# Kernel tuning notes

Measured on AMD Instinct MI355X. Metric: run time of the kernel, lower is better.

The kernel has to match this reference:

```python
import jax, jax.numpy as jnp
import numpy as np

LN_EPS = 1e-5


def _layernorm_2d(x, w, b):
    # LayerNorm over the last two dims (d, d) with elementwise affine.
    mu = jnp.mean(x, axis=(-2, -1), keepdims=True)
    var = jnp.var(x, axis=(-2, -1), keepdims=True)
    return (x - mu) * jax.lax.rsqrt(var + LN_EPS) * w + b


def setup_inputs() -> dict:
    key = jax.random.key(0)
    k_x, k_a, k_w, k_b = jax.random.split(key, 4)
    B, T, D = 2, 512, 64
    x = jax.random.normal(k_x, (B, T, D, D), dtype=jnp.float32)
    log_A = jax.random.normal(k_a, (D,), dtype=jnp.float32) * 0.02
    # dt_proj: nn.Linear(dim, 1) -> weight (1, dim) stored here as (dim,), bias (1,)
    bound = 1.0 / np.sqrt(D)
    dt_w = jax.random.uniform(k_w, (D,), dtype=jnp.float32, minval=-bound, maxval=bound)
    dt_b = jax.random.uniform(k_b, (1,), dtype=jnp.float32, minval=-bound, maxval=bound)
    ln_w = jnp.ones((D, D), dtype=jnp.float32)
    ln_b = jnp.zeros((D, D), dtype=jnp.float32)
    return {"x": x, "log_A": log_A, "dt_w": dt_w, "dt_b": dt_b, "ln_w": ln_w, "ln_b": ln_b}


def reference(x, log_A, dt_w, dt_b, ln_w, ln_b):
    B, T, D, _ = x.shape
    xn = _layernorm_2d(x, ln_w, ln_b)                          # [B,T,D,D]
    A_cont = -jnp.exp(log_A)                                   # [D]
    dt = jax.nn.softplus(jnp.einsum('btrc,c->btr', xn, dt_w) + dt_b)  # [B,T,D]
    log_decay = dt * A_cont                                    # [B,T,D]
    cs = jnp.cumsum(log_decay, axis=1)                         # [B,T,D]
    log_M = cs[:, :, None, :] - cs[:, None, :, :]              # [B,T,T,D]
    idx = jnp.arange(T)
    causal = (idx[:, None] >= idx[None, :])[None, :, :, None]  # [1,T,T,1]
    M = jnp.exp(jnp.where(causal, log_M, -jnp.inf))            # [B,T,T,D]
    out = jnp.einsum('btjr,bjrc->btrc', M, xn)                 # [B,T,D,D]
    return out
```

## Files before the change

kernel.cpp:

```cpp
#include <hip/hip_runtime.h>
#include <math.h>

#define B_SZ 2
#define T_SZ 512
#define D_SZ 64
#define ELEMS 4096

#define NCH2 64
#define CLEN2 8
#define NCG  16

#define DECAY_BYTES ((size_t)B_SZ * D_SZ * T_SZ * 4)
#define M_OFF   DECAY_BYTES
#define R_OFF   (DECAY_BYTES + (size_t)B_SZ * T_SZ * 4)

__global__ __launch_bounds__(256) void ln_dt_kernel(
    const float* __restrict__ x, const float* __restrict__ log_A,
    const float* __restrict__ dt_w, const float* __restrict__ dt_b,
    const float* __restrict__ ln_w, const float* __restrict__ ln_b,
    float* __restrict__ decay_t, float* __restrict__ Mst, float* __restrict__ Rst)
{
    const int bt  = blockIdx.x;
    const int tid = threadIdx.x;
    const size_t base = (size_t)bt * ELEMS;

    float4 v[4];
    float sum = 0.f, sumsq = 0.f;
    const float4* xv4 = reinterpret_cast<const float4*>(x + base);
#pragma unroll
    for (int k = 0; k < 4; ++k) {
        v[k] = xv4[tid + 256 * k];
        sum   += v[k].x + v[k].y + v[k].z + v[k].w;
        sumsq += v[k].x * v[k].x + v[k].y * v[k].y + v[k].z * v[k].z + v[k].w * v[k].w;
    }

    __shared__ float red0[4], red1[4];
#pragma unroll
    for (int off = 32; off; off >>= 1) {
        sum   += __shfl_down(sum, off);
        sumsq += __shfl_down(sumsq, off);
    }
    const int wave = tid >> 6;
    if ((tid & 63) == 0) { red0[wave] = sum; red1[wave] = sumsq; }
    __syncthreads();
    sum   = red0[0] + red0[1] + red0[2] + red0[3];
    sumsq = red1[0] + red1[1] + red1[2] + red1[3];

    const float mu = sum * (1.f / ELEMS);
    const float var = sumsq * (1.f / ELEMS) - mu * mu;
    const float rs = rsqrtf(var + 1e-5f);

    const float4* w4p = reinterpret_cast<const float4*>(ln_w);
    const float4* b4p = reinterpret_cast<const float4*>(ln_b);
    const float4* dw4 = reinterpret_cast<const float4*>(dt_w);
    float dot[4] = {0.f, 0.f, 0.f, 0.f};
#pragma unroll
    for (int k = 0; k < 4; ++k) {
        const int f = tid + 256 * k;
        float4 w4 = w4p[f];
        float4 b4 = b4p[f];
        float4 xn;
        xn.x = (v[k].x - mu) * rs * w4.x + b4.x;
        xn.y = (v[k].y - mu) * rs * w4.y + b4.y;
        xn.z = (v[k].z - mu) * rs * w4.z + b4.z;
        xn.w = (v[k].w - mu) * rs * w4.w + b4.w;
        float4 wv = dw4[f & 15];
        dot[k] += xn.x * wv.x + xn.y * wv.y + xn.z * wv.z + xn.w * wv.w;
    }

#pragma unroll
    for (int m = 1; m <= 8; m <<= 1) {
#pragma unroll
        for (int k = 0; k < 4; ++k) dot[k] += __shfl_xor(dot[k], m);
    }

    if (tid == 0) { Mst[bt] = mu * rs; Rst[bt] = rs; }

    if ((tid & 15) == 0) {
        const int m = tid >> 4;
        const float db = dt_b[0];
        const int b = bt >> 9;
        const int t = bt & (T_SZ - 1);
#pragma unroll
        for (int k = 0; k < 4; ++k) {
            const int r = m + 16 * k;
            const float z = dot[k] + db;
            const float dt = (z > 20.f) ? z : log1pf(expf(z));
            const float A = -expf(log_A[r]);
            decay_t[((size_t)(b * D_SZ + r)) * T_SZ + t] = expf(dt * A);
        }
    }
}

__global__ __launch_bounds__(1024, 1) void scan_row4_kernel(
    const float* __restrict__ x,
    const float* __restrict__ Mst, const float* __restrict__ Rst,
    const float* __restrict__ decay_t,
    const float* __restrict__ ln_w, const float* __restrict__ ln_b,
    float* __restrict__ out)
{
    const int tid = threadIdx.x;
    const int cg  = tid & (NCG - 1);
    const int k   = tid >> 4;
    const int b   = blockIdx.x >> 6;
    const int r   = blockIdx.x & 63;
    const int t0  = k * CLEN2;
    const int c0  = cg * 4;

    __shared__ float  sd[T_SZ];
    __shared__ float  sM[T_SZ];
    __shared__ float  sR[T_SZ];
    __shared__ float4 sS[NCH2][NCG];
    __shared__ float  sP[NCH2];

    if (tid < 128) {
        reinterpret_cast<float4*>(sd)[tid] =
            reinterpret_cast<const float4*>(decay_t + (size_t)blockIdx.x * T_SZ)[tid];
    } else if (tid < 256) {
        const int i = tid - 128;
        reinterpret_cast<float4*>(sM)[i] =
            reinterpret_cast<const float4*>(Mst + b * T_SZ)[i];
    } else if (tid < 384) {
        const int i = tid - 256;
        reinterpret_cast<float4*>(sR)[i] =
            reinterpret_cast<const float4*>(Rst + b * T_SZ)[i];
    }
    const float4 lw = *reinterpret_cast<const float4*>(ln_w + r * D_SZ + c0);
    const float4 lb = *reinterpret_cast<const float4*>(ln_b + r * D_SZ + c0);
    __syncthreads();

    const float* xp = x + ((size_t)(b * T_SZ + t0) * D_SZ + r) * D_SZ + c0;

    float4 v[CLEN2];
    float4 S = make_float4(0.f, 0.f, 0.f, 0.f);
    float  P = 1.f;
#pragma unroll
    for (int i = 0; i < CLEN2; ++i) {
        const float4 xv = *reinterpret_cast<const float4*>(xp + (size_t)i * ELEMS);
        const int   t = t0 + i;
        const float M = sM[t], R = sR[t], d = sd[t];
        const float xn0 = fmaf(fmaf(xv.x, R, -M), lw.x, lb.x);
        const float xn1 = fmaf(fmaf(xv.y, R, -M), lw.y, lb.y);
        const float xn2 = fmaf(fmaf(xv.z, R, -M), lw.z, lb.z);
        const float xn3 = fmaf(fmaf(xv.w, R, -M), lw.w, lb.w);
        S.x = fmaf(S.x, d, xn0);
        S.y = fmaf(S.y, d, xn1);
        S.z = fmaf(S.z, d, xn2);
        S.w = fmaf(S.w, d, xn3);
        P *= d;
        v[i] = S;
    }

    sS[k][cg] = S;
    if (cg == 0) sP[k] = P;
    __syncthreads();

    float4 C = make_float4(0.f, 0.f, 0.f, 0.f);
    for (int j = 0; j < k; ++j) {
        const float  Pj = sP[j];
        const float4 Sj = sS[j][cg];
        C.x = fmaf(Pj, C.x, Sj.x);
        C.y = fmaf(Pj, C.y, Sj.y);
        C.z = fmaf(Pj, C.z, Sj.z);
        C.w = fmaf(Pj, C.w, Sj.w);
    }

    float* op = out + ((size_t)(b * T_SZ + t0) * D_SZ + r) * D_SZ + c0;
    float rp = 1.f;
#pragma unroll
    for (int i = 0; i < CLEN2; ++i) {
        rp *= sd[t0 + i];
        float4 o;
        o.x = fmaf(rp, C.x, v[i].x);
        o.y = fmaf(rp, C.y, v[i].y);
        o.z = fmaf(rp, C.z, v[i].z);
        o.w = fmaf(rp, C.w, v[i].w);
        *reinterpret_cast<float4*>(op + (size_t)i * ELEMS) = o;
    }
}

extern "C" void kernel_launch(void* const* d_in, const int* in_sizes, int n_in,
                              void* d_out, int out_size, void* d_ws, size_t ws_size,
                              hipStream_t stream) {
    const float* x     = (const float*)d_in[0];
    const float* log_A = (const float*)d_in[1];
    const float* dt_w  = (const float*)d_in[2];
    const float* dt_b  = (const float*)d_in[3];
    const float* ln_w  = (const float*)d_in[4];
    const float* ln_b  = (const float*)d_in[5];
    float* out     = (float*)d_out;
    float* decay_t = (float*)d_ws;
    float* Mst     = (float*)((char*)d_ws + M_OFF);
    float* Rst     = (float*)((char*)d_ws + R_OFF);

    ln_dt_kernel<<<B_SZ * T_SZ, 256, 0, stream>>>(
        x, log_A, dt_w, dt_b, ln_w, ln_b, decay_t, Mst, Rst);

    scan_row4_kernel<<<B_SZ * D_SZ, 1024, 0, stream>>>(
        x, Mst, Rst, decay_t, ln_w, ln_b, out);
}
```

Measured before the change: 23.41 us.

## Move dt/decay computation into scan kernel; reduce first kernel to stats only

The first kernel now only computes per-(b,t) LayerNorm mean and rstd, with no ln_w/ln_b/dt_w loads and no decay writes. The scan kernel normalizes x itself, computes the dt dot product with a 16-lane shuffle reduction, applies softplus and exp to get the decay per row, and keeps decays in registers. The x loads are also hoisted ahead of the shared-memory staging so they overlap. This removes the decay workspace round trip and shrinks the first pass, at the cost of extra transcendental and shuffle work inside the latency-bound scan kernel.

```diff
diff --git a/kernel.cpp b/kernel.cpp
--- a/kernel.cpp
+++ b/kernel.cpp
@@ -10,92 +10,51 @@
 #define CLEN2 8
 #define NCG  16
 
-#define DECAY_BYTES ((size_t)B_SZ * D_SZ * T_SZ * 4)
-#define M_OFF   DECAY_BYTES
-#define R_OFF   (DECAY_BYTES + (size_t)B_SZ * T_SZ * 4)
+#define M_OFF 0
+#define R_OFF ((size_t)B_SZ * T_SZ * 4)
 
-__global__ __launch_bounds__(256) void ln_dt_kernel(
-    const float* __restrict__ x, const float* __restrict__ log_A,
-    const float* __restrict__ dt_w, const float* __restrict__ dt_b,
-    const float* __restrict__ ln_w, const float* __restrict__ ln_b,
-    float* __restrict__ decay_t, float* __restrict__ Mst, float* __restrict__ Rst)
+__global__ __launch_bounds__(256) void stats_kernel(
+    const float* __restrict__ x,
+    float* __restrict__ Mst, float* __restrict__ Rst)
 {
     const int bt  = blockIdx.x;
     const int tid = threadIdx.x;
     const size_t base = (size_t)bt * ELEMS;
 
-    float4 v[4];
-    float sum = 0.f, sumsq = 0.f;
+    float sum = 0.f, ssq = 0.f;
     const float4* xv4 = reinterpret_cast<const float4*>(x + base);
 #pragma unroll
     for (int k = 0; k < 4; ++k) {
-        v[k] = xv4[tid + 256 * k];
-        sum   += v[k].x + v[k].y + v[k].z + v[k].w;
-        sumsq += v[k].x * v[k].x + v[k].y * v[k].y + v[k].z * v[k].z + v[k].w * v[k].w;
+        const float4 v = xv4[tid + 256 * k];
+        sum += v.x + v.y + v.z + v.w;
+        ssq += v.x * v.x + v.y * v.y + v.z * v.z + v.w * v.w;
     }
 
     __shared__ float red0[4], red1[4];
 #pragma unroll
     for (int off = 32; off; off >>= 1) {
-        sum   += __shfl_down(sum, off);
-        sumsq += __shfl_down(sumsq, off);
+        sum += __shfl_down(sum, off);
+        ssq += __shfl_down(ssq, off);
     }
     const int wave = tid >> 6;
-    if ((tid & 63) == 0) { red0[wave] = sum; red1[wave] = sumsq; }
+    if ((tid & 63) == 0) { red0[wave] = sum; red1[wave] = ssq; }
     __syncthreads();
-    sum   = red0[0] + red0[1] + red0[2] + red0[3];
-    sumsq = red1[0] + red1[1] + red1[2] + red1[3];
-
-    const float mu = sum * (1.f / ELEMS);
-    const float var = sumsq * (1.f / ELEMS) - mu * mu;
-    const float rs = rsqrtf(var + 1e-5f);
-
-    const float4* w4p = reinterpret_cast<const float4*>(ln_w);
-    const float4* b4p = reinterpret_cast<const float4*>(ln_b);
-    const float4* dw4 = reinterpret_cast<const float4*>(dt_w);
-    float dot[4] = {0.f, 0.f, 0.f, 0.f};
-#pragma unroll
-    for (int k = 0; k < 4; ++k) {
-        const int f = tid + 256 * k;
-        float4 w4 = w4p[f];
-        float4 b4 = b4p[f];
-        float4 xn;
-        xn.x = (v[k].x - mu) * rs * w4.x + b4.x;
-        xn.y = (v[k].y - mu) * rs * w4.y + b4.y;
-        xn.z = (v[k].z - mu) * rs * w4.z + b4.z;
-        xn.w = (v[k].w - mu) * rs * w4.w + b4.w;
-        float4 wv = dw4[f & 15];
-        dot[k] += xn.x * wv.x + xn.y * wv.y + xn.z * wv.z + xn.w * wv.w;
-    }
-
-#pragma unroll
-    for (int m = 1; m <= 8; m <<= 1) {
-#pragma unroll
-        for (int k = 0; k < 4; ++k) dot[k] += __shfl_xor(dot[k], m);
-    }
-
-    if (tid == 0) { Mst[bt] = mu * rs; Rst[bt] = rs; }
-
-    if ((tid & 15) == 0) {
-        const int m = tid >> 4;
-        const float db = dt_b[0];
-        const int b = bt >> 9;
-        const int t = bt & (T_SZ - 1);
-#pragma unroll
-        for (int k = 0; k < 4; ++k) {
-            const int r = m + 16 * k;
-            const float z = dot[k] + db;
-            const float dt = (z > 20.f) ? z : log1pf(expf(z));
-            const float A = -expf(log_A[r]);
-            decay_t[((size_t)(b * D_SZ + r)) * T_SZ + t] = expf(dt * A);
-        }
+    if (tid == 0) {
+        sum = red0[0] + red0[1] + red0[2] + red0[3];
+        ssq = red1[0] + red1[1] + red1[2] + red1[3];
+        const float mu = sum * (1.f / ELEMS);
+        const float var = ssq * (1.f / ELEMS) - mu * mu;
+        const float rs = rsqrtf(var + 1e-5f);
+        Mst[bt] = mu * rs;
+        Rst[bt] = rs;
     }
 }
 
-__global__ __launch_bounds__(1024, 1) void scan_row4_kernel(
+__global__ __launch_bounds__(1024, 1) void scan_full_kernel(
     const float* __restrict__ x,
     const float* __restrict__ Mst, const float* __restrict__ Rst,
-    const float* __restrict__ decay_t,
+    const float* __restrict__ log_A,
+    const float* __restrict__ dt_w, const float* __restrict__ dt_b,
     const float* __restrict__ ln_w, const float* __restrict__ ln_b,
     float* __restrict__ out)
 {
@@ -107,47 +66,64 @@
     const int t0  = k * CLEN2;
     const int c0  = cg * 4;
 
-    __shared__ float  sd[T_SZ];
     __shared__ float  sM[T_SZ];
     __shared__ float  sR[T_SZ];
     __shared__ float4 sS[NCH2][NCG];
     __shared__ float  sP[NCH2];
 
+    const float4 lw = *reinterpret_cast<const float4*>(ln_w + r * D_SZ + c0);
+    const float4 lb = *reinterpret_cast<const float4*>(ln_b + r * D_SZ + c0);
+    const float4 dw = *reinterpret_cast<const float4*>(dt_w + c0);
+    const float  db = dt_b[0];
+    const float  Arow = -expf(log_A[r]);
+
+    const float* xp = x + ((size_t)(b * T_SZ + t0) * D_SZ + r) * D_SZ + c0;
+    float4 v[CLEN2];
+#pragma unroll
+    for (int i = 0; i < CLEN2; ++i)
+        v[i] = *reinterpret_cast<const float4*>(xp + (size_t)i * ELEMS);
+
     if (tid < 128) {
-        reinterpret_cast<float4*>(sd)[tid] =
-            reinterpret_cast<const float4*>(decay_t + (size_t)blockIdx.x * T_SZ)[tid];
+        reinterpret_cast<float4*>(sM)[tid] =
+            reinterpret_cast<const float4*>(Mst + b * T_SZ)[tid];
     } else if (tid < 256) {
         const int i = tid - 128;
-        reinterpret_cast<float4*>(sM)[i] =
-            reinterpret_cast<const float4*>(Mst + b * T_SZ)[i];
-    } else if (tid < 384) {
-        const int i = tid - 256;
         reinterpret_cast<float4*>(sR)[i] =
             reinterpret_cast<const float4*>(Rst + b * T_SZ)[i];
     }
-    const float4 lw = *reinterpret_cast<const float4*>(ln_w + r * D_SZ + c0);
-    const float4 lb = *reinterpret_cast<const float4*>(ln_b + r * D_SZ + c0);
     __syncthreads();
 
-    const float* xp = x + ((size_t)(b * T_SZ + t0) * D_SZ + r) * D_SZ + c0;
-
-    float4 v[CLEN2];
-    float4 S = make_float4(0.f, 0.f, 0.f, 0.f);
-    float  P = 1.f;
+    float d[CLEN2];
 #pragma unroll
     for (int i = 0; i < CLEN2; ++i) {
-        const float4 xv = *reinterpret_cast<const float4*>(xp + (size_t)i * ELEMS);
-        const int   t = t0 + i;
-        const float M = sM[t], R = sR[t], d = sd[t];
-        const float xn0 = fmaf(fmaf(xv.x, R, -M), lw.x, lb.x);
-        const float xn1 = fmaf(fmaf(xv.y, R, -M), lw.y, lb.y);
-        const float xn2 = fmaf(fmaf(xv.z, R, -M), lw.z, lb.z);
-        const float xn3 = fmaf(fmaf(xv.w, R, -M), lw.w, lb.w);
-        S.x = fmaf(S.x, d, xn0);
-        S.y = fmaf(S.y, d, xn1);
-        S.z = fmaf(S.z, d, xn2);
-        S.w = fmaf(S.w, d, xn3);
-        P *= d;
+        const int t = t0 + i;
+        const float M = sM[t], R = sR[t];
+        float4 xn;
+        xn.x = fmaf(fmaf(v[i].x, R, -M), lw.x, lb.x);
+        xn.y = fmaf(fmaf(v[i].y, R, -M), lw.y, lb.y);
+        xn.z = fmaf(fmaf(v[i].z, R, -M), lw.z, lb.z);
+        xn.w = fmaf(fmaf(v[i].w, R, -M), lw.w, lb.w);
+        v[i] = xn;
+        float pd = xn.x * dw.x + xn.y * dw.y + xn.z * dw.z + xn.w * dw.w;
+        pd += __shfl_xor(pd, 1);
+        pd += __shfl_xor(pd, 2);
+        pd += __shfl_xor(pd, 4);
+        pd += __shfl_xor(pd, 8);
+        const float z = pd + db;
+        const float dtv = (z > 20.f) ? z : log1pf(expf(z));
+        d[i] = expf(dtv * Arow);
+    }
+
+    float4 S = make_float4(0.f, 0.f, 0.f, 0.f);
+    float P = 1.f;
+#pragma unroll
+    for (int i = 0; i < CLEN2; ++i) {
+        const float di = d[i];
+        S.x = fmaf(S.x, di, v[i].x);
+        S.y = fmaf(S.y, di, v[i].y);
+        S.z = fmaf(S.z, di, v[i].z);
+        S.w = fmaf(S.w, di, v[i].w);
+        P *= di;
         v[i] = S;
     }
 
@@ -169,7 +145,7 @@
     float rp = 1.f;
 #pragma unroll
     for (int i = 0; i < CLEN2; ++i) {
-        rp *= sd[t0 + i];
+        rp *= d[i];
         float4 o;
         o.x = fmaf(rp, C.x, v[i].x);
         o.y = fmaf(rp, C.y, v[i].y);
@@ -188,14 +164,12 @@
     const float* dt_b  = (const float*)d_in[3];
     const float* ln_w  = (const float*)d_in[4];
     const float* ln_b  = (const float*)d_in[5];
-    float* out     = (float*)d_out;
-    float* decay_t = (float*)d_ws;
-    float* Mst     = (float*)((char*)d_ws + M_OFF);
-    float* Rst     = (float*)((char*)d_ws + R_OFF);
+    float* out = (float*)d_out;
+    float* Mst = (float*)((char*)d_ws + M_OFF);
+    float* Rst = (float*)((char*)d_ws + R_OFF);
 
-    ln_dt_kernel<<<B_SZ * T_SZ, 256, 0, stream>>>(
-        x, log_A, dt_w, dt_b, ln_w, ln_b, decay_t, Mst, Rst);
+    stats_kernel<<<B_SZ * T_SZ, 256, 0, stream>>>(x, Mst, Rst);
 
-    scan_row4_kernel<<<B_SZ * D_SZ, 1024, 0, stream>>>(
-        x, Mst, Rst, decay_t, ln_w, ln_b, out);
+    scan_full_kernel<<<B_SZ * D_SZ, 1024, 0, stream>>>(
+        x, Mst, Rst, log_A, dt_w, dt_b, ln_w, ln_b, out);
 }
```

Result: slower. 25.89 us (+10.6%).

## Split scan rows across column halves and use two-level chunk carry scan

Applied to the files above, without the earlier changes.

The scan kernel now launches two 512-thread blocks per (batch,row), each handling 32 columns, which doubles the block count to fill more CUs. The serial carry loop over up to 63 previous chunks is replaced by a two-level scan: a local scan within groups of 8 chunks, then a scan over group totals. This shortens the longest dependent chain at the cost of an extra barrier and some shared-memory traffic. Each block also reloads the decay/M/R vectors, duplicating those small reads.

```diff
diff --git a/kernel.cpp b/kernel.cpp
--- a/kernel.cpp
+++ b/kernel.cpp
@@ -8,7 +8,7 @@
 
 #define NCH2 64
 #define CLEN2 8
-#define NCG  16
+#define NCG  8
 
 #define DECAY_BYTES ((size_t)B_SZ * D_SZ * T_SZ * 4)
 #define M_OFF   DECAY_BYTES
@@ -92,7 +92,7 @@
     }
 }
 
-__global__ __launch_bounds__(1024, 1) void scan_row4_kernel(
+__global__ __launch_bounds__(512, 2) void scan_hfold_kernel(
     const float* __restrict__ x,
     const float* __restrict__ Mst, const float* __restrict__ Rst,
     const float* __restrict__ decay_t,
@@ -101,21 +101,25 @@
 {
     const int tid = threadIdx.x;
     const int cg  = tid & (NCG - 1);
-    const int k   = tid >> 4;
-    const int b   = blockIdx.x >> 6;
-    const int r   = blockIdx.x & 63;
+    const int k   = tid >> 3;
+    const int ch  = blockIdx.x & 1;
+    const int row = blockIdx.x >> 1;
+    const int b   = row >> 6;
+    const int r   = row & 63;
     const int t0  = k * CLEN2;
-    const int c0  = cg * 4;
+    const int c0  = ch * 32 + cg * 4;
 
     __shared__ float  sd[T_SZ];
     __shared__ float  sM[T_SZ];
     __shared__ float  sR[T_SZ];
     __shared__ float4 sS[NCH2][NCG];
     __shared__ float  sP[NCH2];
+    __shared__ float4 sGS[8][NCG];
+    __shared__ float  sGP[8];
 
     if (tid < 128) {
         reinterpret_cast<float4*>(sd)[tid] =
-            reinterpret_cast<const float4*>(decay_t + (size_t)blockIdx.x * T_SZ)[tid];
+            reinterpret_cast<const float4*>(decay_t + (size_t)row * T_SZ)[tid];
     } else if (tid < 256) {
         const int i = tid - 128;
         reinterpret_cast<float4*>(sM)[i] =
@@ -139,14 +143,10 @@
         const float4 xv = *reinterpret_cast<const float4*>(xp + (size_t)i * ELEMS);
         const int   t = t0 + i;
         const float M = sM[t], R = sR[t], d = sd[t];
-        const float xn0 = fmaf(fmaf(xv.x, R, -M), lw.x, lb.x);
-        const float xn1 = fmaf(fmaf(xv.y, R, -M), lw.y, lb.y);
-        const float xn2 = fmaf(fmaf(xv.z, R, -M), lw.z, lb.z);
-        const float xn3 = fmaf(fmaf(xv.w, R, -M), lw.w, lb.w);
-        S.x = fmaf(S.x, d, xn0);
-        S.y = fmaf(S.y, d, xn1);
-        S.z = fmaf(S.z, d, xn2);
-        S.w = fmaf(S.w, d, xn3);
+        S.x = fmaf(S.x, d, fmaf(fmaf(xv.x, R, -M), lw.x, lb.x));
+        S.y = fmaf(S.y, d, fmaf(fmaf(xv.y, R, -M), lw.y, lb.y));
+        S.z = fmaf(S.z, d, fmaf(fmaf(xv.z, R, -M), lw.z, lb.z));
+        S.w = fmaf(S.w, d, fmaf(fmaf(xv.w, R, -M), lw.w, lb.w));
         P *= d;
         v[i] = S;
     }
@@ -155,15 +155,44 @@
     if (cg == 0) sP[k] = P;
     __syncthreads();
 
-    float4 C = make_float4(0.f, 0.f, 0.f, 0.f);
-    for (int j = 0; j < k; ++j) {
+    const int g = k >> 3;
+    const int g0 = g << 3;
+    float4 L = make_float4(0.f, 0.f, 0.f, 0.f);
+    float  Q = 1.f;
+    for (int j = g0; j < k; ++j) {
         const float  Pj = sP[j];
         const float4 Sj = sS[j][cg];
-        C.x = fmaf(Pj, C.x, Sj.x);
-        C.y = fmaf(Pj, C.y, Sj.y);
-        C.z = fmaf(Pj, C.z, Sj.z);
-        C.w = fmaf(Pj, C.w, Sj.w);
-    }
+        L.x = fmaf(Pj, L.x, Sj.x);
+        L.y = fmaf(Pj, L.y, Sj.y);
+        L.z = fmaf(Pj, L.z, Sj.z);
+        L.w = fmaf(Pj, L.w, Sj.w);
+        Q *= Pj;
+    }
+    if ((k & 7) == 7) {
+        float4 GS;
+        GS.x = fmaf(P, L.x, S.x);
+        GS.y = fmaf(P, L.y, S.y);
+        GS.z = fmaf(P, L.z, S.z);
+        GS.w = fmaf(P, L.w, S.w);
+        sGS[g][cg] = GS;
+        if (cg == 0) sGP[g] = Q * P;
+    }
+    __syncthreads();
+
+    float4 CG = make_float4(0.f, 0.f, 0.f, 0.f);
+    for (int h = 0; h < g; ++h) {
+        const float  Ph = sGP[h];
+        const float4 Sh = sGS[h][cg];
+        CG.x = fmaf(Ph, CG.x, Sh.x);
+        CG.y = fmaf(Ph, CG.y, Sh.y);
+        CG.z = fmaf(Ph, CG.z, Sh.z);
+        CG.w = fmaf(Ph, CG.w, Sh.w);
+    }
+    float4 C;
+    C.x = fmaf(Q, CG.x, L.x);
+    C.y = fmaf(Q, CG.y, L.y);
+    C.z = fmaf(Q, CG.z, L.z);
+    C.w = fmaf(Q, CG.w, L.w);
 
     float* op = out + ((size_t)(b * T_SZ + t0) * D_SZ + r) * D_SZ + c0;
     float rp = 1.f;
@@ -196,6 +225,6 @@
     ln_dt_kernel<<<B_SZ * T_SZ, 256, 0, stream>>>(
         x, log_A, dt_w, dt_b, ln_w, ln_b, decay_t, Mst, Rst);
 
-    scan_row4_kernel<<<B_SZ * D_SZ, 1024, 0, stream>>>(
+    scan_hfold_kernel<<<B_SZ * D_SZ * 2, 512, 0, stream>>>(
         x, Mst, Rst, decay_t, ln_w, ln_b, out);
 }
```

New measurement: 22.75 us. 2.8% less time.
